# Kernel tuning notes

Measured on AMD Instinct MI355X. Metric: run time of the kernel, lower is better.

## Reference

```python
import math
import jax, jax.numpy as jnp
import numpy as np

B, M, N, D, H = 64, 5, 1000, 128, 8
KS = D // H
TANH_CLIP = 10.0

def setup_inputs() -> dict:
    key = jax.random.key(0)
    ks = jax.random.split(key, 12)
    mask = jax.random.randint(ks[8], (B, M, N), 0, 2).astype(bool)
    mask = mask.at[:, 0, 0].set(True)  # guarantee at least one feasible action per batch row
    return {
        'node_embeddings': jax.random.normal(ks[0], (B, N, D), jnp.float32),
        'fixed_context': jax.random.normal(ks[1], (B, 1, D), jnp.float32),
        'prev_node_embeddings': jax.random.normal(ks[2], (B, M, D), jnp.float32),
        'node_dynamic_features': jax.random.normal(ks[3], (B, M, N, 8), jnp.float32),
        'vehicle_dynamic_features': jax.random.normal(ks[4], (B, M, 3), jnp.float32),
        'glimpse_V_static': jax.random.normal(ks[5], (H, B, 1, N, KS), jnp.float32),
        'glimpse_K_static': jax.random.normal(ks[6], (H, B, 1, N, KS), jnp.float32),
        'logit_K_static': jax.random.normal(ks[7], (B, 1, N, D), jnp.float32),
        'feasibility_mask': mask,
        'W_pcv': jax.random.normal(ks[9], (D, D + 3), jnp.float32) * 0.05,
        'W_pns': jax.random.normal(ks[10], (3 * D, 8), jnp.float32) * 0.05,
        'po_weight': jax.random.normal(ks[11], (D, D), jnp.float32) * 0.05,
    }

def reference(node_embeddings, fixed_context, prev_node_embeddings,
              node_dynamic_features, vehicle_dynamic_features,
              glimpse_V_static, glimpse_K_static, logit_K_static,
              feasibility_mask, W_pcv, W_pns, po_weight):
    # current vehicle state projection: [B,M,D]
    cvs = jnp.concatenate([prev_node_embeddings, vehicle_dynamic_features], axis=-1)
    proj_cvs = cvs @ W_pcv.T
    # dynamic node embeddings: [B,M,N,3D] -> three [B,M,N,D] chunks
    nde = node_dynamic_features @ W_pns.T
    gVd, gKd, lKd = jnp.split(nde, 3, axis=-1)
    # make heads: [B,M,N,D] -> [H,B,M,N,KS]
    def mh(x):
        return x.reshape(B, M, N, H, KS).transpose(3, 0, 1, 2, 4)
    glimpse_V = glimpse_V_static + mh(gVd)  # [H,B,M,N,KS]
    glimpse_K = glimpse_K_static + mh(gKd)
    logit_K = logit_K_static + lKd          # [B,M,N,D]
    query = fixed_context + proj_cvs        # [B,M,D]
    Q = query.reshape(B, M, H, KS).transpose(2, 0, 1, 3)  # [H,B,M,KS]
    mask_log = jnp.log(feasibility_mask.astype(jnp.float32))  # [B,M,N]
    compat = jnp.einsum('hbmk,hbmnk->hbmn', Q, glimpse_K) / math.sqrt(KS)
    compat = compat + mask_log[None]
    # softmax over joint vehicle*node axis
    attn = jax.nn.softmax(compat.reshape(H, B, M * N), axis=-1).reshape(H, B, M, N)
    heads = jnp.einsum('hbmn,hbmnk->hbmk', attn, glimpse_V)  # [H,B,M,KS]
    concat = heads.transpose(1, 2, 0, 3).reshape(B, M, D)
    final_Q = concat @ po_weight.T          # [B,M,D]
    logits = jnp.einsum('bmd,bmnd->bmn', final_Q, logit_K) / math.sqrt(D)
    logits = jnp.tanh(logits) * TANH_CLIP + mask_log
    probs = jax.nn.softmax(logits.reshape(B, M * N), axis=-1)
    return probs
```

## Files before the change

### kernel.cpp

```cpp
#include <hip/hip_runtime.h>
#include <cstddef>

#define BB 64
#define MM 5
#define NN 1000
#define DD 128
#define HH 8
#define KSZ 16
#define NCH 4
#define CH2 250
#define NC3 8
#define CH3 125
#define INV_SQRT_D 0.08838834764831845f

__device__ __forceinline__ float tanh_fast(float x) {
  float e = __expf(2.f * x);
  return 1.f - 2.f / (e + 1.f);
}

__global__ __launch_bounds__(256) void k1_query(
    const float* __restrict__ fc, const float* __restrict__ pne,
    const float* __restrict__ vdf, const float* __restrict__ wpcv,
    const float* __restrict__ wpns, const int* __restrict__ mask,
    float* __restrict__ q_ws, float* __restrict__ qw_ws,
    unsigned int* __restrict__ pmask)
{
  const int t = threadIdx.x;
  if (blockIdx.x >= BB * MM) {
    const int b = blockIdx.x - BB * MM;
    const int* mb = mask + (size_t)(b * MM) * NN;
    for (int n = t; n < NN; n += 256) {
      unsigned int pm = 0;
#pragma unroll
      for (int m = 0; m < MM; ++m) pm |= (mb[m * NN + n] != 0 ? 1u : 0u) << m;
      pmask[b * NN + n] = pm;
    }
    return;
  }
  const int bm = blockIdx.x;
  const int b = bm / MM;
  const int k = t & 15, gid = t >> 4;
  __shared__ float qsh[DD];

  float cvr[9];
  const float* pner = pne + (size_t)bm * DD;
#pragma unroll
  for (int jp = 0; jp < 8; ++jp) cvr[jp] = pner[k + 16 * jp];
  cvr[8] = (k < 3) ? vdf[bm * 3 + k] : 0.f;

#pragma unroll 2
  for (int dd = 0; dd < 8; ++dd) {
    const int d = gid + 16 * dd;
    const float* wrow = wpcv + d * 131;
    float p = 0.f;
#pragma unroll
    for (int jp = 0; jp < 8; ++jp) p = fmaf(cvr[jp], wrow[k + 16 * jp], p);
    if (k < 3) p = fmaf(cvr[8], wrow[128 + k], p);
    p += __shfl_xor(p, 1); p += __shfl_xor(p, 2);
    p += __shfl_xor(p, 4); p += __shfl_xor(p, 8);
    if (k == 0) {
      const float q = 0.25f * (p + fc[b * DD + d]);
      qsh[d] = q;
      q_ws[(size_t)bm * DD + d] = q;
    }
  }
  __syncthreads();
  if (t < 64) {
    const int h = t >> 3, f = t & 7;
    float acc = 0.f;
#pragma unroll
    for (int kk = 0; kk < KSZ; ++kk)
      acc = fmaf(qsh[h * KSZ + kk], wpns[(DD + h * KSZ + kk) * 8 + f], acc);
    qw_ws[(b * HH + h) * 40 + (bm % MM) * 8 + f] = acc;
  }
}

__global__ __launch_bounds__(256) void k2_attn(
    const float* __restrict__ ndf, const float* __restrict__ gV,
    const float* __restrict__ gK, const unsigned int* __restrict__ pmask,
    const float* __restrict__ q_ws, const float* __restrict__ qw_ws,
    float* __restrict__ part)
{
  const int blk = blockIdx.x;
  const int c = blk & 3;
  const int h = (blk >> 2) & 7;
  const int b = blk >> 5;
  const int t = threadIdx.x;
  const int k = t & 3, gid = t >> 2;
  const int n0 = c * CH2;

  float4 qr[MM];
  float2 qwr[MM];
#pragma unroll
  for (int m = 0; m < MM; ++m) {
    qr[m] = *(const float4*)(q_ws + (size_t)(b * MM + m) * DD + h * KSZ + 4 * k);
    qwr[m] = *(const float2*)(qw_ws + (b * HH + h) * 40 + m * 8 + 2 * k);
  }
  float4 hacc[MM] = {};
  float2 afv[MM] = {};
  float lsum = 0.f;

  const float* kbase = gK + ((size_t)(h * BB + b) * NN + n0) * KSZ;
  const float* vbase = gV + ((size_t)(h * BB + b) * NN + n0) * KSZ;
  const float* nbase = ndf + ((size_t)(b * MM) * NN + n0) * 8;
  const unsigned int* pmb = pmask + b * NN + n0;

#pragma unroll
  for (int i = 0; i < 4; ++i) {
    const int nl = gid + 64 * i;
    const bool valid = (nl < CH2);
    const int nc = valid ? nl : 0;
    const unsigned int pm = valid ? pmb[nc] : 0u;
    const float4 kv = *(const float4*)(kbase + nc * KSZ + 4 * k);
    const float4 vv = *(const float4*)(vbase + nc * KSZ + 4 * k);
    float2 ndv[MM];
#pragma unroll
    for (int m = 0; m < MM; ++m)
      ndv[m] = *(const float2*)(nbase + ((size_t)m * NN + nc) * 8 + 2 * k);
#pragma unroll
    for (int m = 0; m < MM; ++m) {
      float p = kv.x * qr[m].x + kv.y * qr[m].y + kv.z * qr[m].z + kv.w * qr[m].w
              + ndv[m].x * qwr[m].x + ndv[m].y * qwr[m].y;
      p += __shfl_xor(p, 1); p += __shfl_xor(p, 2);
      const float e = ((pm >> m) & 1u) ? __expf(p) : 0.f;
      hacc[m].x = fmaf(e, vv.x, hacc[m].x);
      hacc[m].y = fmaf(e, vv.y, hacc[m].y);
      hacc[m].z = fmaf(e, vv.z, hacc[m].z);
      hacc[m].w = fmaf(e, vv.w, hacc[m].w);
      afv[m].x = fmaf(e, ndv[m].x, afv[m].x);
      afv[m].y = fmaf(e, ndv[m].y, afv[m].y);
      lsum += e;
    }
  }

#pragma unroll
  for (int m = 0; m < MM; ++m) {
#pragma unroll
    for (int off = 4; off <= 32; off <<= 1) {
      hacc[m].x += __shfl_xor(hacc[m].x, off);
      hacc[m].y += __shfl_xor(hacc[m].y, off);
      hacc[m].z += __shfl_xor(hacc[m].z, off);
      hacc[m].w += __shfl_xor(hacc[m].w, off);
      afv[m].x += __shfl_xor(afv[m].x, off);
      afv[m].y += __shfl_xor(afv[m].y, off);
    }
  }
#pragma unroll
  for (int off = 4; off <= 32; off <<= 1) lsum += __shfl_xor(lsum, off);

  __shared__ float redh[4][MM][KSZ];
  __shared__ float redaf[4][MM][8];
  __shared__ float reds[4];
  const int w = t >> 6;
  if ((t & 63) < 4) {
    const int kk = t & 3;
#pragma unroll
    for (int m = 0; m < MM; ++m) {
      redh[w][m][4 * kk + 0] = hacc[m].x;
      redh[w][m][4 * kk + 1] = hacc[m].y;
      redh[w][m][4 * kk + 2] = hacc[m].z;
      redh[w][m][4 * kk + 3] = hacc[m].w;
      redaf[w][m][2 * kk + 0] = afv[m].x;
      redaf[w][m][2 * kk + 1] = afv[m].y;
    }
  }
  if ((t & 63) == 0) reds[w] = lsum;
  __syncthreads();
  float* P = part + (size_t)blk * 128;
  if (t < 80) {
    const int m = t >> 4, kk = t & 15;
    P[t] = redh[0][m][kk] + redh[1][m][kk] + redh[2][m][kk] + redh[3][m][kk];
  } else if (t < 120) {
    const int r = t - 80, m = r >> 3, f = r & 7;
    P[80 + r] = redaf[0][m][f] + redaf[1][m][f] + redaf[2][m][f] + redaf[3][m][f];
  } else if (t == 120) {
    P[120] = reds[0] + reds[1] + reds[2] + reds[3];
  }
}

__global__ __launch_bounds__(256) void k2b_combine(
    const float* __restrict__ part, const float* __restrict__ wpns,
    const float* __restrict__ po, float* __restrict__ fq_ws,
    float* __restrict__ fw_ws)
{
  const int b = blockIdx.x;
  const int t = threadIdx.x;
  __shared__ float pos[DD][129];
  __shared__ float rgs[HH];
  __shared__ float afs[HH][MM][8];
  __shared__ float cs[MM][DD];
  __shared__ float fqs[MM][DD];

  for (int i = t; i < DD * DD / 4; i += 256) {
    const float4 v = ((const float4*)po)[i];
    const int r = (i * 4) >> 7, cc = (i * 4) & 127;
    pos[r][cc] = v.x; pos[r][cc + 1] = v.y; pos[r][cc + 2] = v.z; pos[r][cc + 3] = v.w;
  }
  const float* pb = part + (size_t)b * 32 * 128;
  if (t < HH) {
    float s = 0.f;
#pragma unroll
    for (int c = 0; c < NCH; ++c) s += pb[(t * 4 + c) * 128 + 120];
    rgs[t] = 1.f / s;
  }
  for (int idx = t; idx < HH * MM * 8; idx += 256) {
    const int h = idx / 40, r = idx % 40;
    float a = 0.f;
#pragma unroll
    for (int c = 0; c < NCH; ++c) a += pb[(h * 4 + c) * 128 + 80 + r];
    afs[h][r >> 3][r & 7] = a;
  }
  __syncthreads();
  for (int idx = t; idx < MM * DD; idx += 256) {
    const int m = idx >> 7, d = idx & 127, h = d >> 4;
    float a = 0.f;
#pragma unroll
    for (int c = 0; c < NCH; ++c) a += pb[(h * 4 + c) * 128 + m * 16 + (d & 15)];
    float cf = 0.f;
#pragma unroll
    for (int f = 0; f < 8; ++f) cf = fmaf(wpns[d * 8 + f], afs[h][m][f], cf);
    cs[m][d] = (a + cf) * rgs[h];
  }
  __syncthreads();
  for (int idx = t; idx < MM * DD; idx += 256) {
    const int m = idx >> 7, d = idx & 127;
    float acc = 0.f;
#pragma unroll 8
    for (int j = 0; j < DD; ++j) acc = fmaf(cs[m][j], pos[d][j], acc);
    acc *= INV_SQRT_D;
    fqs[m][d] = acc;
    fq_ws[(size_t)b * (MM * DD) + idx] = acc;
  }
  __syncthreads();
  if (t < MM * 8) {
    const int m = t >> 3, f = t & 7;
    float acc = 0.f;
#pragma unroll 16
    for (int d = 0; d < DD; ++d) acc = fmaf(fqs[m][d], wpns[(2 * DD + d) * 8 + f], acc);
    fw_ws[b * 40 + t] = acc;
  }
}

__global__ __launch_bounds__(512) void k3_logits(
    const float* __restrict__ ndf, const float* __restrict__ lK,
    const unsigned int* __restrict__ pmask, const float* __restrict__ fq_ws,
    const float* __restrict__ fw_ws, float* __restrict__ out,
    float* __restrict__ stats)
{
  const int b = blockIdx.x >> 3;
  const int c = blockIdx.x & 7;
  const int t = threadIdx.x;
  const int k = t & 15, gid = t >> 4;
  const int n0 = c * CH3;

  float4 fqr[MM][2];
  float fwr[MM];
#pragma unroll
  for (int m = 0; m < MM; ++m) {
    fqr[m][0] = *(const float4*)(fq_ws + (size_t)(b * MM + m) * DD + 8 * k);
    fqr[m][1] = *(const float4*)(fq_ws + (size_t)(b * MM + m) * DD + 8 * k + 4);
    fwr[m] = fw_ws[b * 40 + m * 8 + (k & 7)];
  }
  float lsum = 0.f;

#pragma unroll
  for (int i = 0; i < 4; ++i) {
    const int nl = gid + 32 * i;
    const bool valid = (nl < CH3);
    const int n = n0 + (valid ? nl : 0);
    const unsigned int pm = valid ? pmask[b * NN + n] : 0u;
    const float* lkr = lK + ((size_t)b * NN + n) * DD;
    const float4 l0 = *(const float4*)(lkr + 8 * k);
    const float4 l1 = *(const float4*)(lkr + 8 * k + 4);
    float ndv[MM];
#pragma unroll
    for (int m = 0; m < MM; ++m)
      ndv[m] = (k < 8) ? ndf[((size_t)(b * MM + m) * NN + n) * 8 + k] : 0.f;
#pragma unroll
    for (int m = 0; m < MM; ++m) {
      float p = l0.x * fqr[m][0].x + l0.y * fqr[m][0].y
              + l0.z * fqr[m][0].z + l0.w * fqr[m][0].w
              + l1.x * fqr[m][1].x + l1.y * fqr[m][1].y
              + l1.z * fqr[m][1].z + l1.w * fqr[m][1].w
              + ndv[m] * fwr[m];
      p += __shfl_xor(p, 1); p += __shfl_xor(p, 2);
      p += __shfl_xor(p, 4); p += __shfl_xor(p, 8);
      const float e = ((pm >> m) & 1u) ? __expf(tanh_fast(p) * 10.f) : 0.f;
      if (valid) {
        lsum += e;
        if (k == 0) out[(size_t)(b * MM + m) * NN + n] = e;
      }
    }
  }
  lsum += __shfl_xor(lsum, 16);
  lsum += __shfl_xor(lsum, 32);
  __shared__ float wred[8];
  if ((t & 63) == 0) wred[t >> 6] = lsum;
  __syncthreads();
  if (t == 0) {
    float s = 0.f;
#pragma unroll
    for (int w = 0; w < 8; ++w) s += wred[w];
    stats[b * NC3 + c] = s;
  }
}

__global__ __launch_bounds__(256) void k4_probs(
    const float* __restrict__ stats, float* __restrict__ out)
{
  const int bm = blockIdx.x;
  const int b = bm / MM;
  const int t = threadIdx.x;
  float s = 0.f;
#pragma unroll
  for (int c = 0; c < NC3; ++c) s += stats[b * NC3 + c];
  const float scale = 1.f / s;
  if (t < 250) {
    float4* p = (float4*)(out + (size_t)bm * NN);
    float4 v = p[t];
    v.x *= scale; v.y *= scale; v.z *= scale; v.w *= scale;
    p[t] = v;
  }
}

extern "C" void kernel_launch(void* const* d_in, const int* in_sizes, int n_in,
                              void* d_out, int out_size, void* d_ws, size_t ws_size,
                              hipStream_t stream) {
  const float* fc   = (const float*)d_in[1];
  const float* pne  = (const float*)d_in[2];
  const float* ndf  = (const float*)d_in[3];
  const float* vdf  = (const float*)d_in[4];
  const float* gV   = (const float*)d_in[5];
  const float* gK   = (const float*)d_in[6];
  const float* lK   = (const float*)d_in[7];
  const int*   mask = (const int*)d_in[8];
  const float* wpcv = (const float*)d_in[9];
  const float* wpns = (const float*)d_in[10];
  const float* po   = (const float*)d_in[11];

  float* q_ws  = (float*)d_ws;
  float* qw_ws = q_ws + BB * MM * DD;
  float* part  = qw_ws + BB * HH * MM * 8;
  float* fq_ws = part + (size_t)BB * HH * NCH * 128;
  float* fw_ws = fq_ws + BB * MM * DD;
  float* stats = fw_ws + BB * 40;
  unsigned int* pmask = (unsigned int*)(stats + BB * NC3);
  float* out   = (float*)d_out;

  k1_query<<<BB * MM + BB, 256, 0, stream>>>(fc, pne, vdf, wpcv, wpns, mask,
                                             q_ws, qw_ws, pmask);
  k2_attn<<<BB * HH * NCH, 256, 0, stream>>>(ndf, gV, gK, pmask, q_ws, qw_ws, part);
  k2b_combine<<<BB, 256, 0, stream>>>(part, wpns, po, fq_ws, fw_ws);
  k3_logits<<<BB * NC3, 512, 0, stream>>>(ndf, lK, pmask, fq_ws, fw_ws, out, stats);
  k4_probs<<<BB * MM, 256, 0, stream>>>(stats, out);
}
```

Before: 58.85 us.

## Fuse combine stage into logits kernel and batch attention loads up front

The per-batch combine kernel is removed. Each of the 8 logits blocks per batch now recomputes the attention head reduction and the output projection into shared memory before computing logits, which drops one launch and the global round trip of the final query. In the attention kernel, all K, V and node-feature loads are issued ahead of the compute loop, and a minimum-blocks hint is added to the launch bounds, to expose more memory-level parallelism. The trade is 8x redundant loading of the 128x128 projection matrix and redundant matvec work per batch, plus about 70KB of shared memory per logits block, which may reduce occupancy.

```diff
diff --git a/kernel.cpp b/kernel.cpp
--- a/kernel.cpp
+++ b/kernel.cpp
@@ -75,7 +75,7 @@
   }
 }
 
-__global__ __launch_bounds__(256) void k2_attn(
+__global__ __launch_bounds__(256, 3) void k2_attn(
     const float* __restrict__ ndf, const float* __restrict__ gV,
     const float* __restrict__ gK, const unsigned int* __restrict__ pmask,
     const float* __restrict__ q_ws, const float* __restrict__ qw_ws,
@@ -89,46 +89,53 @@
   const int k = t & 3, gid = t >> 2;
   const int n0 = c * CH2;
 
-  float4 qr[MM];
-  float2 qwr[MM];
-#pragma unroll
-  for (int m = 0; m < MM; ++m) {
-    qr[m] = *(const float4*)(q_ws + (size_t)(b * MM + m) * DD + h * KSZ + 4 * k);
-    qwr[m] = *(const float2*)(qw_ws + (b * HH + h) * 40 + m * 8 + 2 * k);
-  }
-  float4 hacc[MM] = {};
-  float2 afv[MM] = {};
-  float lsum = 0.f;
-
   const float* kbase = gK + ((size_t)(h * BB + b) * NN + n0) * KSZ;
   const float* vbase = gV + ((size_t)(h * BB + b) * NN + n0) * KSZ;
   const float* nbase = ndf + ((size_t)(b * MM) * NN + n0) * 8;
   const unsigned int* pmb = pmask + b * NN + n0;
 
+  float4 kv[4], vv[4];
+  float2 ndv[4][MM];
+  unsigned int pm[4];
 #pragma unroll
   for (int i = 0; i < 4; ++i) {
     const int nl = gid + 64 * i;
     const bool valid = (nl < CH2);
     const int nc = valid ? nl : 0;
-    const unsigned int pm = valid ? pmb[nc] : 0u;
-    const float4 kv = *(const float4*)(kbase + nc * KSZ + 4 * k);
-    const float4 vv = *(const float4*)(vbase + nc * KSZ + 4 * k);
-    float2 ndv[MM];
+    pm[i] = valid ? pmb[nc] : 0u;
+    kv[i] = *(const float4*)(kbase + nc * KSZ + 4 * k);
+    vv[i] = *(const float4*)(vbase + nc * KSZ + 4 * k);
 #pragma unroll
     for (int m = 0; m < MM; ++m)
-      ndv[m] = *(const float2*)(nbase + ((size_t)m * NN + nc) * 8 + 2 * k);
+      ndv[i][m] = *(const float2*)(nbase + ((size_t)m * NN + nc) * 8 + 2 * k);
+  }
+
+  float4 qr[MM];
+  float2 qwr[MM];
+#pragma unroll
+  for (int m = 0; m < MM; ++m) {
+    qr[m] = *(const float4*)(q_ws + (size_t)(b * MM + m) * DD + h * KSZ + 4 * k);
+    qwr[m] = *(const float2*)(qw_ws + (b * HH + h) * 40 + m * 8 + 2 * k);
+  }
+  float4 hacc[MM] = {};
+  float2 afv[MM] = {};
+  float lsum = 0.f;
+
+#pragma unroll
+  for (int i = 0; i < 4; ++i) {
 #pragma unroll
     for (int m = 0; m < MM; ++m) {
-      float p = kv.x * qr[m].x + kv.y * qr[m].y + kv.z * qr[m].z + kv.w * qr[m].w
-              + ndv[m].x * qwr[m].x + ndv[m].y * qwr[m].y;
+      float p = kv[i].x * qr[m].x + kv[i].y * qr[m].y
+              + kv[i].z * qr[m].z + kv[i].w * qr[m].w
+              + ndv[i][m].x * qwr[m].x + ndv[i][m].y * qwr[m].y;
       p += __shfl_xor(p, 1); p += __shfl_xor(p, 2);
-      const float e = ((pm >> m) & 1u) ? __expf(p) : 0.f;
-      hacc[m].x = fmaf(e, vv.x, hacc[m].x);
-      hacc[m].y = fmaf(e, vv.y, hacc[m].y);
-      hacc[m].z = fmaf(e, vv.z, hacc[m].z);
-      hacc[m].w = fmaf(e, vv.w, hacc[m].w);
-      afv[m].x = fmaf(e, ndv[m].x, afv[m].x);
-      afv[m].y = fmaf(e, ndv[m].y, afv[m].y);
+      const float e = ((pm[i] >> m) & 1u) ? __expf(p) : 0.f;
+      hacc[m].x = fmaf(e, vv[i].x, hacc[m].x);
+      hacc[m].y = fmaf(e, vv[i].y, hacc[m].y);
+      hacc[m].z = fmaf(e, vv[i].z, hacc[m].z);
+      hacc[m].w = fmaf(e, vv[i].w, hacc[m].w);
+      afv[m].x = fmaf(e, ndv[i][m].x, afv[m].x);
+      afv[m].y = fmaf(e, ndv[i][m].y, afv[m].y);
       lsum += e;
     }
   }
@@ -178,20 +185,25 @@
   }
 }
 
-__global__ __launch_bounds__(256) void k2b_combine(
-    const float* __restrict__ part, const float* __restrict__ wpns,
-    const float* __restrict__ po, float* __restrict__ fq_ws,
-    float* __restrict__ fw_ws)
+__global__ __launch_bounds__(512) void k3_logits(
+    const float* __restrict__ ndf, const float* __restrict__ lK,
+    const unsigned int* __restrict__ pmask, const float* __restrict__ part,
+    const float* __restrict__ wpns, const float* __restrict__ po,
+    float* __restrict__ out, float* __restrict__ stats)
 {
-  const int b = blockIdx.x;
+  const int b = blockIdx.x >> 3;
+  const int c = blockIdx.x & 7;
   const int t = threadIdx.x;
+
   __shared__ float pos[DD][129];
   __shared__ float rgs[HH];
   __shared__ float afs[HH][MM][8];
   __shared__ float cs[MM][DD];
   __shared__ float fqs[MM][DD];
-
-  for (int i = t; i < DD * DD / 4; i += 256) {
+  __shared__ float fw[MM][8];
+  __shared__ float wred[8];
+
+  for (int i = t; i < DD * DD / 4; i += 512) {
     const float4 v = ((const float4*)po)[i];
     const int r = (i * 4) >> 7, cc = (i * 4) & 127;
     pos[r][cc] = v.x; pos[r][cc + 1] = v.y; pos[r][cc + 2] = v.z; pos[r][cc + 3] = v.w;
@@ -200,36 +212,34 @@
   if (t < HH) {
     float s = 0.f;
 #pragma unroll
-    for (int c = 0; c < NCH; ++c) s += pb[(t * 4 + c) * 128 + 120];
+    for (int cc = 0; cc < NCH; ++cc) s += pb[(t * 4 + cc) * 128 + 120];
     rgs[t] = 1.f / s;
   }
-  for (int idx = t; idx < HH * MM * 8; idx += 256) {
-    const int h = idx / 40, r = idx % 40;
+  if (t < HH * MM * 8) {
+    const int h = t / 40, r = t % 40;
     float a = 0.f;
 #pragma unroll
-    for (int c = 0; c < NCH; ++c) a += pb[(h * 4 + c) * 128 + 80 + r];
+    for (int cc = 0; cc < NCH; ++cc) a += pb[(h * 4 + cc) * 128 + 80 + r];
     afs[h][r >> 3][r & 7] = a;
   }
   __syncthreads();
-  for (int idx = t; idx < MM * DD; idx += 256) {
+  for (int idx = t; idx < MM * DD; idx += 512) {
     const int m = idx >> 7, d = idx & 127, h = d >> 4;
     float a = 0.f;
 #pragma unroll
-    for (int c = 0; c < NCH; ++c) a += pb[(h * 4 + c) * 128 + m * 16 + (d & 15)];
+    for (int cc = 0; cc < NCH; ++cc) a += pb[(h * 4 + cc) * 128 + m * 16 + (d & 15)];
     float cf = 0.f;
 #pragma unroll
     for (int f = 0; f < 8; ++f) cf = fmaf(wpns[d * 8 + f], afs[h][m][f], cf);
     cs[m][d] = (a + cf) * rgs[h];
   }
   __syncthreads();
-  for (int idx = t; idx < MM * DD; idx += 256) {
+  for (int idx = t; idx < MM * DD; idx += 512) {
     const int m = idx >> 7, d = idx & 127;
     float acc = 0.f;
 #pragma unroll 8
     for (int j = 0; j < DD; ++j) acc = fmaf(cs[m][j], pos[d][j], acc);
-    acc *= INV_SQRT_D;
-    fqs[m][d] = acc;
-    fq_ws[(size_t)b * (MM * DD) + idx] = acc;
+    fqs[m][d] = acc * INV_SQRT_D;
   }
   __syncthreads();
   if (t < MM * 8) {
@@ -237,29 +247,19 @@
     float acc = 0.f;
 #pragma unroll 16
     for (int d = 0; d < DD; ++d) acc = fmaf(fqs[m][d], wpns[(2 * DD + d) * 8 + f], acc);
-    fw_ws[b * 40 + t] = acc;
-  }
-}
-
-__global__ __launch_bounds__(512) void k3_logits(
-    const float* __restrict__ ndf, const float* __restrict__ lK,
-    const unsigned int* __restrict__ pmask, const float* __restrict__ fq_ws,
-    const float* __restrict__ fw_ws, float* __restrict__ out,
-    float* __restrict__ stats)
-{
-  const int b = blockIdx.x >> 3;
-  const int c = blockIdx.x & 7;
-  const int t = threadIdx.x;
+    fw[m][f] = acc;
+  }
+  __syncthreads();
+
   const int k = t & 15, gid = t >> 4;
   const int n0 = c * CH3;
-
   float4 fqr[MM][2];
   float fwr[MM];
 #pragma unroll
   for (int m = 0; m < MM; ++m) {
-    fqr[m][0] = *(const float4*)(fq_ws + (size_t)(b * MM + m) * DD + 8 * k);
-    fqr[m][1] = *(const float4*)(fq_ws + (size_t)(b * MM + m) * DD + 8 * k + 4);
-    fwr[m] = fw_ws[b * 40 + m * 8 + (k & 7)];
+    fqr[m][0] = *(const float4*)(&fqs[m][8 * k]);
+    fqr[m][1] = *(const float4*)(&fqs[m][8 * k + 4]);
+    fwr[m] = fw[m][k & 7];
   }
   float lsum = 0.f;
 
@@ -294,7 +294,6 @@
   }
   lsum += __shfl_xor(lsum, 16);
   lsum += __shfl_xor(lsum, 32);
-  __shared__ float wred[8];
   if ((t & 63) == 0) wred[t >> 6] = lsum;
   __syncthreads();
   if (t == 0) {
@@ -341,16 +340,13 @@
   float* q_ws  = (float*)d_ws;
   float* qw_ws = q_ws + BB * MM * DD;
   float* part  = qw_ws + BB * HH * MM * 8;
-  float* fq_ws = part + (size_t)BB * HH * NCH * 128;
-  float* fw_ws = fq_ws + BB * MM * DD;
-  float* stats = fw_ws + BB * 40;
+  float* stats = part + (size_t)BB * HH * NCH * 128;
   unsigned int* pmask = (unsigned int*)(stats + BB * NC3);
   float* out   = (float*)d_out;
 
   k1_query<<<BB * MM + BB, 256, 0, stream>>>(fc, pne, vdf, wpcv, wpns, mask,
                                              q_ws, qw_ws, pmask);
   k2_attn<<<BB * HH * NCH, 256, 0, stream>>>(ndf, gV, gK, pmask, q_ws, qw_ws, part);
-  k2b_combine<<<BB, 256, 0, stream>>>(part, wpns, po, fq_ws, fw_ws);
-  k3_logits<<<BB * NC3, 512, 0, stream>>>(ndf, lK, pmask, fq_ws, fw_ws, out, stats);
+  k3_logits<<<BB * NC3, 512, 0, stream>>>(ndf, lK, pmask, part, wpns, po, out, stats);
   k4_probs<<<BB * MM, 256, 0, stream>>>(stats, out);
 }
```

Measured after the change: 56.99 us. -3.2%, faster.

## Restructure attention kernel to cover all heads per block with LDS-staged features

Applied to the files above, without the earlier changes.

The attention kernel now gives each 512-thread block all eight heads for one batch and one node chunk. The shared dynamic node features and feasibility mask are staged once in LDS instead of being reloaded by every head, and per-head partials are reduced with LDS atomics. The query kernel is regridded so each block handles a quarter of the output dimension for all vehicles. The logits kernel uses more, smaller 256-thread blocks. Together these aim to cut redundant global traffic and raise parallelism, at the cost of LDS atomics, more partial sums to combine, and a block-wide sync before the main loop.

```diff
diff --git a/kernel.cpp b/kernel.cpp
--- a/kernel.cpp
+++ b/kernel.cpp
@@ -7,10 +7,10 @@
 #define DD 128
 #define HH 8
 #define KSZ 16
-#define NCH 4
-#define CH2 250
-#define NC3 8
-#define CH3 125
+#define NCH 8
+#define CH2 125
+#define NC3 16
+#define CH3 63
 #define INV_SQRT_D 0.08838834764831845f
 
 __device__ __forceinline__ float tanh_fast(float x) {
@@ -26,8 +26,8 @@
     unsigned int* __restrict__ pmask)
 {
   const int t = threadIdx.x;
-  if (blockIdx.x >= BB * MM) {
-    const int b = blockIdx.x - BB * MM;
+  if (blockIdx.x >= BB * 4) {
+    const int b = blockIdx.x - BB * 4;
     const int* mb = mask + (size_t)(b * MM) * NN;
     for (int n = t; n < NN; n += 256) {
       unsigned int pm = 0;
@@ -37,20 +37,24 @@
     }
     return;
   }
-  const int bm = blockIdx.x;
-  const int b = bm / MM;
+  const int b = blockIdx.x >> 2;
+  const int dq = blockIdx.x & 3;
   const int k = t & 15, gid = t >> 4;
-  __shared__ float qsh[DD];
+  __shared__ float qsh[MM][32];
 
   float cvr[9];
-  const float* pner = pne + (size_t)bm * DD;
-#pragma unroll
-  for (int jp = 0; jp < 8; ++jp) cvr[jp] = pner[k + 16 * jp];
-  cvr[8] = (k < 3) ? vdf[bm * 3 + k] : 0.f;
-
-#pragma unroll 2
-  for (int dd = 0; dd < 8; ++dd) {
-    const int d = gid + 16 * dd;
+  int curm = -1;
+  for (int r = 0; r < 10; ++r) {
+    const int m = r >> 1;
+    if (m != curm) {
+      curm = m;
+      const float* pner = pne + (size_t)(b * MM + m) * DD;
+#pragma unroll
+      for (int jp = 0; jp < 8; ++jp) cvr[jp] = pner[k + 16 * jp];
+      cvr[8] = (k < 3) ? vdf[(b * MM + m) * 3 + k] : 0.f;
+    }
+    const int dl = (r & 1) * 16 + gid;
+    const int d = dq * 32 + dl;
     const float* wrow = wpcv + d * 131;
     float p = 0.f;
 #pragma unroll
@@ -60,34 +64,50 @@
     p += __shfl_xor(p, 4); p += __shfl_xor(p, 8);
     if (k == 0) {
       const float q = 0.25f * (p + fc[b * DD + d]);
-      qsh[d] = q;
-      q_ws[(size_t)bm * DD + d] = q;
-    }
-  }
-  __syncthreads();
-  if (t < 64) {
-    const int h = t >> 3, f = t & 7;
+      qsh[m][dl] = q;
+      q_ws[(size_t)(b * MM + m) * DD + d] = q;
+    }
+  }
+  __syncthreads();
+  if (t < 80) {
+    const int hh = t / 40;
+    const int r = t - hh * 40, m = r >> 3, f = r & 7;
+    const int h = dq * 2 + hh;
     float acc = 0.f;
 #pragma unroll
     for (int kk = 0; kk < KSZ; ++kk)
-      acc = fmaf(qsh[h * KSZ + kk], wpns[(DD + h * KSZ + kk) * 8 + f], acc);
-    qw_ws[(b * HH + h) * 40 + (bm % MM) * 8 + f] = acc;
-  }
-}
-
-__global__ __launch_bounds__(256) void k2_attn(
+      acc = fmaf(qsh[m][hh * 16 + kk], wpns[(DD + h * KSZ + kk) * 8 + f], acc);
+    qw_ws[(b * HH + h) * 40 + m * 8 + f] = acc;
+  }
+}
+
+__global__ __launch_bounds__(512, 4) void k2_attn(
     const float* __restrict__ ndf, const float* __restrict__ gV,
     const float* __restrict__ gK, const unsigned int* __restrict__ pmask,
     const float* __restrict__ q_ws, const float* __restrict__ qw_ws,
     float* __restrict__ part)
 {
-  const int blk = blockIdx.x;
-  const int c = blk & 3;
-  const int h = (blk >> 2) & 7;
-  const int b = blk >> 5;
-  const int t = threadIdx.x;
-  const int k = t & 3, gid = t >> 2;
+  const int b = blockIdx.x & 63;
+  const int c = blockIdx.x >> 6;
+  const int t = threadIdx.x;
+  const int k = t & 3;
+  const int h = (t >> 2) & 7;
+  const int s = t >> 5;
   const int n0 = c * CH2;
+
+  __shared__ float nlds[CH2][MM][8];
+  __shared__ unsigned int pmlds[CH2];
+  __shared__ float pP[HH][128];
+
+  for (int i = t; i < CH2 * MM * 2; i += 512) {
+    const int m = i / 250;
+    const int r = i - m * 250;
+    const int n = r >> 1, jj = r & 1;
+    const float4 v = *(const float4*)(ndf + ((size_t)(b * MM + m) * NN + n0 + n) * 8 + 4 * jj);
+    *(float4*)(&nlds[n][m][4 * jj]) = v;
+  }
+  for (int i = t; i < CH2; i += 512) pmlds[i] = pmask[b * NN + n0 + i];
+  for (int i = t; i < HH * 128; i += 512) pP[i >> 7][i & 127] = 0.f;
 
   float4 qr[MM];
   float2 qwr[MM];
@@ -96,86 +116,67 @@
     qr[m] = *(const float4*)(q_ws + (size_t)(b * MM + m) * DD + h * KSZ + 4 * k);
     qwr[m] = *(const float2*)(qw_ws + (b * HH + h) * 40 + m * 8 + 2 * k);
   }
+  __syncthreads();
+
+  const float* kb = gK + ((size_t)(h * BB + b) * NN + n0) * KSZ + 4 * k;
+  const float* vb = gV + ((size_t)(h * BB + b) * NN + n0) * KSZ + 4 * k;
+
   float4 hacc[MM] = {};
   float2 afv[MM] = {};
   float lsum = 0.f;
 
-  const float* kbase = gK + ((size_t)(h * BB + b) * NN + n0) * KSZ;
-  const float* vbase = gV + ((size_t)(h * BB + b) * NN + n0) * KSZ;
-  const float* nbase = ndf + ((size_t)(b * MM) * NN + n0) * 8;
-  const unsigned int* pmb = pmask + b * NN + n0;
-
-#pragma unroll
-  for (int i = 0; i < 4; ++i) {
-    const int nl = gid + 64 * i;
-    const bool valid = (nl < CH2);
-    const int nc = valid ? nl : 0;
-    const unsigned int pm = valid ? pmb[nc] : 0u;
-    const float4 kv = *(const float4*)(kbase + nc * KSZ + 4 * k);
-    const float4 vv = *(const float4*)(vbase + nc * KSZ + 4 * k);
-    float2 ndv[MM];
-#pragma unroll
-    for (int m = 0; m < MM; ++m)
-      ndv[m] = *(const float2*)(nbase + ((size_t)m * NN + nc) * 8 + 2 * k);
+#pragma unroll
+  for (int i = 0; i < 8; ++i) {
+    const int nl = s + 16 * i;
+    if (nl < CH2) {
+      const float4 kv = *(const float4*)(kb + nl * KSZ);
+      const float4 vv = *(const float4*)(vb + nl * KSZ);
+      const unsigned int pm = pmlds[nl];
+#pragma unroll
+      for (int m = 0; m < MM; ++m) {
+        const float2 nd = *(const float2*)(&nlds[nl][m][2 * k]);
+        float p = kv.x * qr[m].x + kv.y * qr[m].y
+                + kv.z * qr[m].z + kv.w * qr[m].w
+                + nd.x * qwr[m].x + nd.y * qwr[m].y;
+        p += __shfl_xor(p, 1); p += __shfl_xor(p, 2);
+        const float e = ((pm >> m) & 1u) ? __expf(p) : 0.f;
+        hacc[m].x = fmaf(e, vv.x, hacc[m].x);
+        hacc[m].y = fmaf(e, vv.y, hacc[m].y);
+        hacc[m].z = fmaf(e, vv.z, hacc[m].z);
+        hacc[m].w = fmaf(e, vv.w, hacc[m].w);
+        afv[m].x = fmaf(e, nd.x, afv[m].x);
+        afv[m].y = fmaf(e, nd.y, afv[m].y);
+        lsum += e;
+      }
+    }
+  }
+
+#pragma unroll
+  for (int m = 0; m < MM; ++m) {
+    hacc[m].x += __shfl_xor(hacc[m].x, 32);
+    hacc[m].y += __shfl_xor(hacc[m].y, 32);
+    hacc[m].z += __shfl_xor(hacc[m].z, 32);
+    hacc[m].w += __shfl_xor(hacc[m].w, 32);
+    afv[m].x += __shfl_xor(afv[m].x, 32);
+    afv[m].y += __shfl_xor(afv[m].y, 32);
+  }
+  lsum += __shfl_xor(lsum, 32);
+
+  if ((t & 63) < 32) {
 #pragma unroll
     for (int m = 0; m < MM; ++m) {
-      float p = kv.x * qr[m].x + kv.y * qr[m].y + kv.z * qr[m].z + kv.w * qr[m].w
-              + ndv[m].x * qwr[m].x + ndv[m].y * qwr[m].y;
-      p += __shfl_xor(p, 1); p += __shfl_xor(p, 2);
-      const float e = ((pm >> m) & 1u) ? __expf(p) : 0.f;
-      hacc[m].x = fmaf(e, vv.x, hacc[m].x);
-      hacc[m].y = fmaf(e, vv.y, hacc[m].y);
-      hacc[m].z = fmaf(e, vv.z, hacc[m].z);
-      hacc[m].w = fmaf(e, vv.w, hacc[m].w);
-      afv[m].x = fmaf(e, ndv[m].x, afv[m].x);
-      afv[m].y = fmaf(e, ndv[m].y, afv[m].y);
-      lsum += e;
-    }
-  }
-
-#pragma unroll
-  for (int m = 0; m < MM; ++m) {
-#pragma unroll
-    for (int off = 4; off <= 32; off <<= 1) {
-      hacc[m].x += __shfl_xor(hacc[m].x, off);
-      hacc[m].y += __shfl_xor(hacc[m].y, off);
-      hacc[m].z += __shfl_xor(hacc[m].z, off);
-      hacc[m].w += __shfl_xor(hacc[m].w, off);
-      afv[m].x += __shfl_xor(afv[m].x, off);
-      afv[m].y += __shfl_xor(afv[m].y, off);
-    }
-  }
-#pragma unroll
-  for (int off = 4; off <= 32; off <<= 1) lsum += __shfl_xor(lsum, off);
-
-  __shared__ float redh[4][MM][KSZ];
-  __shared__ float redaf[4][MM][8];
-  __shared__ float reds[4];
-  const int w = t >> 6;
-  if ((t & 63) < 4) {
-    const int kk = t & 3;
-#pragma unroll
-    for (int m = 0; m < MM; ++m) {
-      redh[w][m][4 * kk + 0] = hacc[m].x;
-      redh[w][m][4 * kk + 1] = hacc[m].y;
-      redh[w][m][4 * kk + 2] = hacc[m].z;
-      redh[w][m][4 * kk + 3] = hacc[m].w;
-      redaf[w][m][2 * kk + 0] = afv[m].x;
-      redaf[w][m][2 * kk + 1] = afv[m].y;
-    }
-  }
-  if ((t & 63) == 0) reds[w] = lsum;
-  __syncthreads();
-  float* P = part + (size_t)blk * 128;
-  if (t < 80) {
-    const int m = t >> 4, kk = t & 15;
-    P[t] = redh[0][m][kk] + redh[1][m][kk] + redh[2][m][kk] + redh[3][m][kk];
-  } else if (t < 120) {
-    const int r = t - 80, m = r >> 3, f = r & 7;
-    P[80 + r] = redaf[0][m][f] + redaf[1][m][f] + redaf[2][m][f] + redaf[3][m][f];
-  } else if (t == 120) {
-    P[120] = reds[0] + reds[1] + reds[2] + reds[3];
-  }
+      atomicAdd(&pP[h][m * 16 + 4 * k + 0], hacc[m].x);
+      atomicAdd(&pP[h][m * 16 + 4 * k + 1], hacc[m].y);
+      atomicAdd(&pP[h][m * 16 + 4 * k + 2], hacc[m].z);
+      atomicAdd(&pP[h][m * 16 + 4 * k + 3], hacc[m].w);
+      atomicAdd(&pP[h][80 + m * 8 + 2 * k + 0], afv[m].x);
+      atomicAdd(&pP[h][80 + m * 8 + 2 * k + 1], afv[m].y);
+    }
+    if (k == 0) atomicAdd(&pP[h][120], lsum);
+  }
+  __syncthreads();
+  float* P = part + (size_t)(b * NCH + c) * HH * 128;
+  for (int i = t; i < HH * 128; i += 512) P[i] = pP[i >> 7][i & 127];
 }
 
 __global__ __launch_bounds__(256) void k2b_combine(
@@ -196,18 +197,18 @@
     const int r = (i * 4) >> 7, cc = (i * 4) & 127;
     pos[r][cc] = v.x; pos[r][cc + 1] = v.y; pos[r][cc + 2] = v.z; pos[r][cc + 3] = v.w;
   }
-  const float* pb = part + (size_t)b * 32 * 128;
+  const float* pb = part + (size_t)b * NCH * HH * 128;
   if (t < HH) {
     float s = 0.f;
 #pragma unroll
-    for (int c = 0; c < NCH; ++c) s += pb[(t * 4 + c) * 128 + 120];
+    for (int c = 0; c < NCH; ++c) s += pb[(c * HH + t) * 128 + 120];
     rgs[t] = 1.f / s;
   }
   for (int idx = t; idx < HH * MM * 8; idx += 256) {
     const int h = idx / 40, r = idx % 40;
     float a = 0.f;
 #pragma unroll
-    for (int c = 0; c < NCH; ++c) a += pb[(h * 4 + c) * 128 + 80 + r];
+    for (int c = 0; c < NCH; ++c) a += pb[(c * HH + h) * 128 + 80 + r];
     afs[h][r >> 3][r & 7] = a;
   }
   __syncthreads();
@@ -215,7 +216,7 @@
     const int m = idx >> 7, d = idx & 127, h = d >> 4;
     float a = 0.f;
 #pragma unroll
-    for (int c = 0; c < NCH; ++c) a += pb[(h * 4 + c) * 128 + m * 16 + (d & 15)];
+    for (int c = 0; c < NCH; ++c) a += pb[(c * HH + h) * 128 + m * 16 + (d & 15)];
     float cf = 0.f;
 #pragma unroll
     for (int f = 0; f < 8; ++f) cf = fmaf(wpns[d * 8 + f], afs[h][m][f], cf);
@@ -241,14 +242,14 @@
   }
 }
 
-__global__ __launch_bounds__(512) void k3_logits(
+__global__ __launch_bounds__(256) void k3_logits(
     const float* __restrict__ ndf, const float* __restrict__ lK,
     const unsigned int* __restrict__ pmask, const float* __restrict__ fq_ws,
     const float* __restrict__ fw_ws, float* __restrict__ out,
     float* __restrict__ stats)
 {
-  const int b = blockIdx.x >> 3;
-  const int c = blockIdx.x & 7;
+  const int b = blockIdx.x & 63;
+  const int c = blockIdx.x >> 6;
   const int t = threadIdx.x;
   const int k = t & 15, gid = t >> 4;
   const int n0 = c * CH3;
@@ -265,17 +266,18 @@
 
 #pragma unroll
   for (int i = 0; i < 4; ++i) {
-    const int nl = gid + 32 * i;
-    const bool valid = (nl < CH3);
-    const int n = n0 + (valid ? nl : 0);
-    const unsigned int pm = valid ? pmask[b * NN + n] : 0u;
-    const float* lkr = lK + ((size_t)b * NN + n) * DD;
+    const int nl = gid + 16 * i;
+    const int n = n0 + nl;
+    const bool valid = (nl < CH3) && (n < NN);
+    const int nc = valid ? n : n0;
+    const unsigned int pm = valid ? pmask[b * NN + nc] : 0u;
+    const float* lkr = lK + ((size_t)b * NN + nc) * DD;
     const float4 l0 = *(const float4*)(lkr + 8 * k);
     const float4 l1 = *(const float4*)(lkr + 8 * k + 4);
     float ndv[MM];
 #pragma unroll
     for (int m = 0; m < MM; ++m)
-      ndv[m] = (k < 8) ? ndf[((size_t)(b * MM + m) * NN + n) * 8 + k] : 0.f;
+      ndv[m] = (k < 8) ? ndf[((size_t)(b * MM + m) * NN + nc) * 8 + k] : 0.f;
 #pragma unroll
     for (int m = 0; m < MM; ++m) {
       float p = l0.x * fqr[m][0].x + l0.y * fqr[m][0].y
@@ -288,21 +290,17 @@
       const float e = ((pm >> m) & 1u) ? __expf(tanh_fast(p) * 10.f) : 0.f;
       if (valid) {
         lsum += e;
-        if (k == 0) out[(size_t)(b * MM + m) * NN + n] = e;
+        if (k == 0) out[(size_t)(b * MM + m) * NN + nc] = e;
       }
     }
   }
   lsum += __shfl_xor(lsum, 16);
   lsum += __shfl_xor(lsum, 32);
-  __shared__ float wred[8];
+  __shared__ float wred[4];
   if ((t & 63) == 0) wred[t >> 6] = lsum;
   __syncthreads();
-  if (t == 0) {
-    float s = 0.f;
-#pragma unroll
-    for (int w = 0; w < 8; ++w) s += wred[w];
-    stats[b * NC3 + c] = s;
-  }
+  if (t == 0)
+    stats[b * NC3 + c] = wred[0] + wred[1] + wred[2] + wred[3];
 }
 
 __global__ __launch_bounds__(256) void k4_probs(
@@ -340,17 +338,17 @@
 
   float* q_ws  = (float*)d_ws;
   float* qw_ws = q_ws + BB * MM * DD;
-  float* part  = qw_ws + BB * HH * MM * 8;
-  float* fq_ws = part + (size_t)BB * HH * NCH * 128;
+  float* part  = qw_ws + BB * HH * 40;
+  float* fq_ws = part + (size_t)BB * NCH * HH * 128;
   float* fw_ws = fq_ws + BB * MM * DD;
   float* stats = fw_ws + BB * 40;
   unsigned int* pmask = (unsigned int*)(stats + BB * NC3);
   float* out   = (float*)d_out;
 
-  k1_query<<<BB * MM + BB, 256, 0, stream>>>(fc, pne, vdf, wpcv, wpns, mask,
-                                             q_ws, qw_ws, pmask);
-  k2_attn<<<BB * HH * NCH, 256, 0, stream>>>(ndf, gV, gK, pmask, q_ws, qw_ws, part);
+  k1_query<<<BB * 4 + BB, 256, 0, stream>>>(fc, pne, vdf, wpcv, wpns, mask,
+                                            q_ws, qw_ws, pmask);
+  k2_attn<<<BB * NCH, 512, 0, stream>>>(ndf, gV, gK, pmask, q_ws, qw_ws, part);
   k2b_combine<<<BB, 256, 0, stream>>>(part, wpns, po, fq_ws, fw_ws);
-  k3_logits<<<BB * NC3, 512, 0, stream>>>(ndf, lK, pmask, fq_ws, fw_ws, out, stats);
+  k3_logits<<<BB * NC3, 256, 0, stream>>>(ndf, lK, pmask, fq_ws, fw_ws, out, stats);
   k4_probs<<<BB * MM, 256, 0, stream>>>(stats, out);
 }
```

After: 81.03 us. +37.7%, slower.
